# Kernel tuning notes

Hardware: AMD Instinct MI355X
Metric: run time of the kernel (lower is better)

The kernel has to match this reference:

```python
import jax, jax.numpy as jnp
import numpy as np

N = 100000      # nodes
E = 1600000     # edges
G = 2000        # molecules (graphs)
F = 40          # node features
FE = 16         # edge features
H = 64          # conv width
HM = 128        # mlp width
C = 2           # classes
NEG_SLOPE = 0.01
BN_EPS = 1e-5


def leaky(x):
    return jnp.where(x >= 0, x, NEG_SLOPE * x)


def batch_norm(x, g, b):
    # training-mode BatchNorm over the node axis (biased variance, eps=1e-5)
    m = jnp.mean(x, axis=0)
    v = jnp.var(x, axis=0)
    return (x - m) * jax.lax.rsqrt(v + BN_EPS) * g + b


def setup_inputs() -> dict:
    key = jax.random.key(0)
    ks = iter(jax.random.split(key, 100))

    def nrm(shape, s=1.0):
        return jax.random.normal(next(ks), shape, dtype=jnp.float32) * s

    inp = {}
    inp["x"] = nrm((N, F))
    inp["edge_index"] = jax.random.randint(next(ks), (2, E), 0, N, dtype=jnp.int32)
    inp["edge_attr"] = nrm((E, FE))
    inp["batch"] = jnp.repeat(jnp.arange(G, dtype=jnp.int32), N // G)

    dims = [(F, H), (H, H), (H, H)]
    for i, (ci, co) in enumerate(dims):
        inp[f"conv{i}_eps"] = jnp.zeros((1,), dtype=jnp.float32)
        inp[f"conv{i}_We"] = nrm((FE, ci), 1.0 / np.sqrt(FE))
        inp[f"conv{i}_be"] = nrm((ci,), 0.05)
        inp[f"conv{i}_W1"] = nrm((ci, co), 1.0 / np.sqrt(ci))
        inp[f"conv{i}_b1"] = nrm((co,), 0.05)
        inp[f"conv{i}_g1"] = 1.0 + nrm((co,), 0.05)
        inp[f"conv{i}_bt1"] = nrm((co,), 0.05)
        inp[f"conv{i}_W2"] = nrm((co, co), 1.0 / np.sqrt(co))
        inp[f"conv{i}_b2"] = nrm((co,), 0.05)
        inp[f"bn{i}_g"] = 1.0 + nrm((co,), 0.05)
        inp[f"bn{i}_b"] = nrm((co,), 0.05)

    inp["mlp0_W"] = nrm((2 * H, HM), 1.0 / np.sqrt(2 * H))
    inp["mlp0_b"] = nrm((HM,), 0.05)
    inp["mlp1_W"] = nrm((HM, HM), 1.0 / np.sqrt(HM))
    inp["mlp1_b"] = nrm((HM,), 0.05)
    inp["final_W"] = nrm((HM, C), 1.0 / np.sqrt(HM))
    inp["final_b"] = nrm((C,), 0.05)
    return inp


def _forward(x, edge_attr, edge_index, batch, convs, mlps, final_W, final_b):
    src, dst = edge_index[0], edge_index[1]
    for (eps, We, be, W1, b1, g1, bt1, W2, b2, bg, bb) in convs:
        # GINEConv: msg = relu(x_src + lin_edge(edge_attr)); scatter-add to dst
        e = edge_attr @ We + be                    # [E, in]
        msg = jax.nn.relu(x[src] + e)              # gather + fuse
        agg = jax.ops.segment_sum(msg, dst, num_segments=x.shape[0])
        h = (1.0 + eps) * x + agg
        # conv nn: Linear -> BatchNorm -> LeakyReLU -> Linear
        h = batch_norm(h @ W1 + b1, g1, bt1)
        h = leaky(h) @ W2 + b2
        # outer BatchNorm + LeakyReLU
        x = leaky(batch_norm(h, bg, bb))
    # global_add_pool then repeat_interleave by per-mol counts == pool[batch]
    pool = jax.ops.segment_sum(x, batch, num_segments=G)
    x = jnp.concatenate([x, pool[batch]], axis=1)  # [N, 2H]
    for (W, b) in mlps:
        x = leaky(x @ W + b)  # dropout is identity in eval mode
    return x @ final_W + final_b


def reference(x, edge_index, edge_attr, batch,
              conv0_eps, conv0_We, conv0_be, conv0_W1, conv0_b1, conv0_g1, conv0_bt1, conv0_W2, conv0_b2, bn0_g, bn0_b,
              conv1_eps, conv1_We, conv1_be, conv1_W1, conv1_b1, conv1_g1, conv1_bt1, conv1_W2, conv1_b2, bn1_g, bn1_b,
              conv2_eps, conv2_We, conv2_be, conv2_W1, conv2_b1, conv2_g1, conv2_bt1, conv2_W2, conv2_b2, bn2_g, bn2_b,
              mlp0_W, mlp0_b, mlp1_W, mlp1_b, final_W, final_b):
    convs = [
        (conv0_eps, conv0_We, conv0_be, conv0_W1, conv0_b1, conv0_g1, conv0_bt1, conv0_W2, conv0_b2, bn0_g, bn0_b),
        (conv1_eps, conv1_We, conv1_be, conv1_W1, conv1_b1, conv1_g1, conv1_bt1, conv1_W2, conv1_b2, bn1_g, bn1_b),
        (conv2_eps, conv2_We, conv2_be, conv2_W1, conv2_b1, conv2_g1, conv2_bt1, conv2_W2, conv2_b2, bn2_g, bn2_b),
    ]
    mlps = [(mlp0_W, mlp0_b), (mlp1_W, mlp1_b)]
    return _forward(x, edge_attr, edge_index, batch, convs, mlps, final_W, final_b)
```

## Files before the change

kernel.cpp:

```cpp
#include <hip/hip_runtime.h>


#define N_  100000
#define E_  1600000
#define G_  2000
#define SCAN_NB 196
#define NBLK 1563

__device__ __forceinline__ float leaky_(float z) { return z >= 0.f ? z : 0.01f * z; }

__global__ __launch_bounds__(256) void hist_kernel(
    const int* __restrict__ dst, int* __restrict__ cur)
{
    for (int e = blockIdx.x * 256 + threadIdx.x; e < E_; e += gridDim.x * 256)
        atomicAdd(&cur[dst[e]], 1);
}

__global__ __launch_bounds__(256) void scanA(
    const int* __restrict__ cur, int* __restrict__ blocksum)
{
    __shared__ int s[256];
    const int t = threadIdx.x, b = blockIdx.x;
    const int i0 = (b * 256 + t) * 2;
    int v = 0;
    if (i0 < N_) v += cur[i0];
    if (i0 + 1 < N_) v += cur[i0 + 1];
    s[t] = v; __syncthreads();
    for (int o = 128; o > 0; o >>= 1) { if (t < o) s[t] += s[t + o]; __syncthreads(); }
    if (t == 0) blocksum[b] = s[0];
}

__global__ __launch_bounds__(256) void scanB(
    const int* __restrict__ blocksum, int* __restrict__ blockpref)
{
    __shared__ int s[256];
    const int t = threadIdx.x;
    int v = (t < SCAN_NB) ? blocksum[t] : 0;
    s[t] = v; __syncthreads();
    for (int o = 1; o < 256; o <<= 1) {
        int u = (t >= o) ? s[t - o] : 0;
        __syncthreads(); s[t] += u; __syncthreads();
    }
    blockpref[t] = s[t] - v;
}

__global__ __launch_bounds__(256) void scanC(
    int* __restrict__ cur, int* __restrict__ off,
    const int* __restrict__ blockpref)
{
    __shared__ int s[256];
    const int t = threadIdx.x, b = blockIdx.x;
    const int i0 = (b * 256 + t) * 2;
    int v0 = (i0 < N_) ? cur[i0] : 0;
    int v1 = (i0 + 1 < N_) ? cur[i0 + 1] : 0;
    int pv = v0 + v1;
    s[t] = pv; __syncthreads();
    for (int o = 1; o < 256; o <<= 1) {
        int u = (t >= o) ? s[t - o] : 0;
        __syncthreads(); s[t] += u; __syncthreads();
    }
    int run = blockpref[b] + s[t] - pv;
    if (i0 < N_) {
        off[i0] = run; cur[i0] = run; run += v0;
        if (i0 + 1 < N_) { off[i0 + 1] = run; cur[i0 + 1] = run; }
    }
    if (b == 0 && t == 0) off[N_] = E_;
}

__global__ __launch_bounds__(256) void scatter_kernel(
    const int* __restrict__ src, const int* __restrict__ dst,
    int* __restrict__ cur, int* __restrict__ src_s, int* __restrict__ eid_s)
{
    for (int e = blockIdx.x * 256 + threadIdx.x; e < E_; e += gridDim.x * 256) {
        int p = atomicAdd(&cur[dst[e]], 1);
        src_s[p] = src[e];
        eid_s[p] = e;
    }
}

__global__ __launch_bounds__(256) void reorder_ea(
    const float* __restrict__ edge_attr, const int* __restrict__ eid_s,
    float4* __restrict__ ea_s)
{
    for (int t = blockIdx.x * 256 + threadIdx.x; t < E_ * 4; t += gridDim.x * 256) {
        int p = t >> 2, q = t & 3;
        int e = eid_s[p];
        ea_s[t] = ((const float4*)edge_attr)[e * 4 + q];
    }
}

#define DPW 13
#define CHUNK 32

template<int CI>
__global__ __launch_bounds__(256, 4) void agg_sorted(
    const float* __restrict__ ea_s,
    const int* __restrict__ src_s,
    const int* __restrict__ off,
    const float* __restrict__ We, const float* __restrict__ be,
    const float* __restrict__ x, float* __restrict__ agg)
{
    __shared__ __align__(16) float s_ea[4][2][CHUNK * 16];
    __shared__ int s_src[4][2][CHUNK];
    const int t = threadIdx.x;
    const int lane = t & 63;
    const int w = t >> 6;
    const int wid = __builtin_amdgcn_readfirstlane(blockIdx.x * 4 + w);

    float wcol[16];
#pragma unroll
    for (int k = 0; k < 16; ++k) wcol[k] = 0.f;
    float beL = 0.f;
    if (lane < CI) {
#pragma unroll
        for (int k = 0; k < 16; ++k) wcol[k] = We[k * CI + lane];
        beL = be[lane];
    }
    const int ln = (lane < CI) ? lane : 0;

    const int d0 = wid * DPW;
    if (d0 >= N_) return;
    const int d1 = min(d0 + DPW, N_);
    const int pw0 = off[d0];
    const int pw1 = off[d1];

    int d = d0;
    int e1 = off[d0 + 1];
    float acc = 0.f;
    int buf = 0;

    {
        const int m4 = min(CHUNK, pw1 - pw0) * 4;
#pragma unroll
        for (int j = 0; j < 2; ++j) {
            const int f = lane + 64 * j;
            float4 v = make_float4(0.f, 0.f, 0.f, 0.f);
            if (f < m4) v = *(const float4*)&ea_s[(size_t)pw0 * 16 + f * 4];
            *(float4*)&s_ea[w][0][f * 4] = v;
        }
        if (lane < CHUNK) {
            const int m = min(CHUNK, pw1 - pw0);
            s_src[w][0][lane] = (lane < m) ? src_s[pw0 + lane] : 0;
        }
    }
    __builtin_amdgcn_wave_barrier();

    for (int cp = pw0; cp < pw1; cp += CHUNK) {
        const int m = min(CHUNK, pw1 - cp);
        const int np = cp + CHUNK;
        const int nm = min(CHUNK, pw1 - np);

        float4 pre0 = make_float4(0.f, 0.f, 0.f, 0.f), pre1 = pre0;
        int psrc = 0;
        if (nm > 0) {
            { int f = lane;      if (f < nm * 4) pre0 = *(const float4*)&ea_s[(size_t)np * 16 + f * 4]; }
            { int f = lane + 64; if (f < nm * 4) pre1 = *(const float4*)&ea_s[(size_t)np * 16 + f * 4]; }
            if (lane < nm) psrc = src_s[np + lane];
        }

        float xr[CHUNK];
#pragma unroll
        for (int i = 0; i < CHUNK; ++i) {
            const int s = s_src[w][buf][i];
            xr[i] = x[(size_t)s * CI + ln];
        }

#pragma unroll
        for (int i = 0; i < CHUNK; ++i) {
            if (i >= m) break;
            while (cp + i == e1) {
                if (lane < CI) agg[(size_t)d * CI + lane] = acc;
                acc = 0.f; ++d;
                e1 = off[d + 1];
            }
            const float* er = &s_ea[w][buf][i * 16];
            float dotv = beL;
#pragma unroll
            for (int k = 0; k < 16; k += 4) {
                float4 ev = *(const float4*)&er[k];
                dotv += ev.x * wcol[k] + ev.y * wcol[k + 1]
                      + ev.z * wcol[k + 2] + ev.w * wcol[k + 3];
            }
            float mm = xr[i] + dotv;
            acc += (mm > 0.f ? mm : 0.f);
        }

        if (nm > 0) {
            *(float4*)&s_ea[w][buf ^ 1][lane * 4] = pre0;
            *(float4*)&s_ea[w][buf ^ 1][(lane + 64) * 4] = pre1;
            if (lane < CHUNK) s_src[w][buf ^ 1][lane] = psrc;
        }
        __builtin_amdgcn_wave_barrier();
        buf ^= 1;
    }

    while (d < d1) {
        if (lane < CI) agg[(size_t)d * CI + lane] = acc;
        acc = 0.f; ++d;
    }
}

template<int CI, int MODE>
__global__ __launch_bounds__(256, 4) void node_gemm(
    const float* __restrict__ in,
    const float* __restrict__ agg,
    const float* __restrict__ eps,
    const float* __restrict__ g1,
    const float* __restrict__ bt1,
    const float* __restrict__ stIn,
    const float* __restrict__ W, const float* __restrict__ bias_,
    float* __restrict__ outbuf, float* __restrict__ partial)
{
    __shared__ __align__(16) float a_lds[64][CI + 4];
    __shared__ __align__(16) float w_lds[CI][68];
    __shared__ float s_sc[64], s_sh[64];
    const int t = threadIdx.x;
    const int n0 = blockIdx.x * 64;
    constexpr int QR = CI / 4;

    if (MODE == 1) {
        if (t < 64) {
            float mean = stIn[t] * (1.0f / N_);
            float var  = stIn[64 + t] * (1.0f / N_) - mean * mean;
            float sc = g1[t] * rsqrtf(var + 1e-5f);
            s_sc[t] = sc;
            s_sh[t] = bt1[t] - mean * sc;
        }
        __syncthreads();
    }

    if (MODE == 0) {
        const float hs = 1.0f + eps[0];
        for (int f = t; f < 64 * QR; f += 256) {
            int i = f / QR, q = f - i * QR;
            int n = n0 + i;
            float4 val = make_float4(0.f, 0.f, 0.f, 0.f);
            if (n < N_) {
                float4 xa = *(const float4*)&in[(size_t)n * CI + q * 4];
                float4 ag = *(const float4*)&agg[(size_t)n * CI + q * 4];
                val = make_float4(hs * xa.x + ag.x, hs * xa.y + ag.y,
                                  hs * xa.z + ag.z, hs * xa.w + ag.w);
            }
            *(float4*)&a_lds[i][q * 4] = val;
        }
    } else {
        for (int f = t; f < 64 * QR; f += 256) {
            int i = f / QR, q = f - i * QR;
            int n = n0 + i;
            float4 val = make_float4(0.f, 0.f, 0.f, 0.f);
            if (n < N_) {
                float4 uv = *(const float4*)&in[(size_t)n * CI + q * 4];
                int c = q * 4;
                val = make_float4(leaky_(uv.x * s_sc[c]     + s_sh[c]),
                                  leaky_(uv.y * s_sc[c + 1] + s_sh[c + 1]),
                                  leaky_(uv.z * s_sc[c + 2] + s_sh[c + 2]),
                                  leaky_(uv.w * s_sc[c + 3] + s_sh[c + 3]));
            }
            *(float4*)&a_lds[i][q * 4] = val;
        }
    }
    for (int f = t; f < CI * 16; f += 256) {
        int k = f >> 4, cq = f & 15;
        *(float4*)&w_lds[k][cq * 4] = *(const float4*)&W[k * 64 + cq * 4];
    }
    __syncthreads();

    const int tr = t & 15;
    const int c0 = (t >> 4) * 4;
    float acc[4][4] = {};
#pragma unroll 2
    for (int k = 0; k < CI; k += 4) {
        float ar[4][4];
#pragma unroll
        for (int j = 0; j < 4; ++j)
            *(float4*)&ar[j][0] = *(const float4*)&a_lds[tr + 16 * j][k];
#pragma unroll
        for (int kk = 0; kk < 4; ++kk) {
            float4 b = *(const float4*)&w_lds[k + kk][c0];
#pragma unroll
            for (int j = 0; j < 4; ++j) {
                acc[j][0] += ar[j][kk] * b.x;
                acc[j][1] += ar[j][kk] * b.y;
                acc[j][2] += ar[j][kk] * b.z;
                acc[j][3] += ar[j][kk] * b.w;
            }
        }
    }

    const float4 bb = *(const float4*)&bias_[c0];
    const float bias[4] = { bb.x, bb.y, bb.z, bb.w };
    float ls[4] = {}, lq[4] = {};
#pragma unroll
    for (int j = 0; j < 4; ++j) {
        int n = n0 + tr + 16 * j;
        if (n < N_) {
            float o[4];
#pragma unroll
            for (int cc = 0; cc < 4; ++cc) {
                o[cc] = acc[j][cc] + bias[cc];
                ls[cc] += o[cc];
                lq[cc] += o[cc] * o[cc];
            }
            *(float4*)&outbuf[(size_t)n * 64 + c0] = make_float4(o[0], o[1], o[2], o[3]);
        }
    }
#pragma unroll
    for (int m = 1; m <= 8; m <<= 1) {
#pragma unroll
        for (int cc = 0; cc < 4; ++cc) {
            ls[cc] += __shfl_xor(ls[cc], m);
            lq[cc] += __shfl_xor(lq[cc], m);
        }
    }
    if (tr == 0) {
#pragma unroll
        for (int cc = 0; cc < 4; ++cc) {
            partial[(size_t)(c0 + cc) * NBLK + blockIdx.x]      = ls[cc];
            partial[(size_t)(64 + c0 + cc) * NBLK + blockIdx.x] = lq[cc];
        }
    }
}

__global__ __launch_bounds__(256) void finalize_stats(
    const float* __restrict__ partial, float* __restrict__ stats)
{
    const int c = blockIdx.x;
    const int t = threadIdx.x;
    float s = 0.f;
    for (int b = t; b < NBLK; b += 256) s += partial[(size_t)c * NBLK + b];
    __shared__ float red[256];
    red[t] = s; __syncthreads();
    for (int o = 128; o > 0; o >>= 1) { if (t < o) red[t] += red[t + o]; __syncthreads(); }
    if (t == 0) stats[c] = red[0];
}

__global__ __launch_bounds__(256) void apply_bn_leaky(
    const float* __restrict__ v, const float* __restrict__ st,
    const float* __restrict__ g, const float* __restrict__ b,
    float* __restrict__ xout)
{
    size_t idx = ((size_t)blockIdx.x * 256 + threadIdx.x) * 4;
    if (idx >= (size_t)N_ * 64) return;
    int c0 = (int)(idx & 63);
    float4 vv = *(const float4*)&v[idx];
    float vi[4] = { vv.x, vv.y, vv.z, vv.w };
    float o[4];
#pragma unroll
    for (int cc = 0; cc < 4; ++cc) {
        int c = c0 + cc;
        float mean = st[c] * (1.0f / N_);
        float var  = st[64 + c] * (1.0f / N_) - mean * mean;
        float sc = g[c] * rsqrtf(var + 1e-5f);
        float sh = b[c] - mean * sc;
        o[cc] = leaky_(vi[cc] * sc + sh);
    }
    *(float4*)&xout[idx] = make_float4(o[0], o[1], o[2], o[3]);
}

__global__ __launch_bounds__(256) void pool_kernel(
    const float* __restrict__ x, float* __restrict__ pool)
{
    const int c = threadIdx.x & 63;
    const int g = blockIdx.x * 4 + (threadIdx.x >> 6);
    const float* p = x + (size_t)g * 50 * 64 + c;
    float s = 0.f;
#pragma unroll
    for (int j = 0; j < 50; ++j) s += p[(size_t)j * 64];
    pool[(size_t)g * 64 + c] = s;
}

__global__ __launch_bounds__(256) void pool_mlp0(
    const float* __restrict__ pool, const float* __restrict__ W0,
    const float* __restrict__ b0, float* __restrict__ g0)
{
    const int t = threadIdx.x;
    const int g = blockIdx.x * 2 + (t >> 7);
    const int c = t & 127;
    float s = b0[c];
    const float* pr = pool + (size_t)g * 64;
#pragma unroll 4
    for (int k = 0; k < 64; ++k)
        s += pr[k] * W0[(size_t)(64 + k) * 128 + c];
    g0[(size_t)g * 128 + c] = s;
}

__global__ __launch_bounds__(256, 2) void mlp_kernel(
    const float* __restrict__ x, const float* __restrict__ g0,
    const float* __restrict__ W0,
    const float* __restrict__ W1, const float* __restrict__ b1,
    const float* __restrict__ Wf, const float* __restrict__ bf,
    float* __restrict__ out)
{
    __shared__ __align__(16) float a_lds[128][132];
    __shared__ __align__(16) float w_lds[16][132];
    __shared__ __align__(16) float sWfT[2][128];
    __shared__ int sbid[128];
    const int t = threadIdx.x;
    const int n0 = blockIdx.x * 128;

    for (int f = t; f < 128 * 16; f += 256) {
        int i = f >> 4, q = f & 15;
        int n = n0 + i;
        float4 val = make_float4(0.f, 0.f, 0.f, 0.f);
        if (n < N_) val = *(const float4*)&x[(size_t)n * 64 + q * 4];
        *(float4*)&a_lds[i][q * 4] = val;
    }
    if (t < 128) {
        int n = n0 + t;
        sbid[t] = (n < N_) ? (n / 50) : (G_ - 1);
        sWfT[0][t] = Wf[t * 2];
        sWfT[1][t] = Wf[t * 2 + 1];
    }

    const int tr = t & 15;
    const int c0 = (t >> 4) * 8;
    float acc[8][8];

#pragma unroll
    for (int j = 0; j < 8; ++j)
#pragma unroll
        for (int cc = 0; cc < 8; ++cc) acc[j][cc] = 0.f;

    for (int kc = 0; kc < 64; kc += 16) {
        __syncthreads();
        for (int f = t; f < 16 * 32; f += 256) {
            int k = f >> 5, cq = f & 31;
            *(float4*)&w_lds[k][cq * 4] = *(const float4*)&W0[(size_t)(kc + k) * 128 + cq * 4];
        }
        __syncthreads();
        for (int k = 0; k < 16; k += 4) {
            float ar[8][4];
#pragma unroll
            for (int j = 0; j < 8; ++j)
                *(float4*)&ar[j][0] = *(const float4*)&a_lds[tr + 16 * j][kc + k];
#pragma unroll
            for (int kk = 0; kk < 4; ++kk) {
                float4 bA = *(const float4*)&w_lds[k + kk][c0];
                float4 bB = *(const float4*)&w_lds[k + kk][c0 + 4];
#pragma unroll
                for (int j = 0; j < 8; ++j) {
                    acc[j][0] += ar[j][kk] * bA.x;
                    acc[j][1] += ar[j][kk] * bA.y;
                    acc[j][2] += ar[j][kk] * bA.z;
                    acc[j][3] += ar[j][kk] * bA.w;
                    acc[j][4] += ar[j][kk] * bB.x;
                    acc[j][5] += ar[j][kk] * bB.y;
                    acc[j][6] += ar[j][kk] * bB.z;
                    acc[j][7] += ar[j][kk] * bB.w;
                }
            }
        }
    }
    __syncthreads();
#pragma unroll
    for (int j = 0; j < 8; ++j) {
        int row = tr + 16 * j;
        const float* gr = g0 + (size_t)sbid[row] * 128;
        float4 gA = *(const float4*)&gr[c0];
        float4 gB = *(const float4*)&gr[c0 + 4];
        float o[8] = { acc[j][0] + gA.x, acc[j][1] + gA.y, acc[j][2] + gA.z, acc[j][3] + gA.w,
                       acc[j][4] + gB.x, acc[j][5] + gB.y, acc[j][6] + gB.z, acc[j][7] + gB.w };
#pragma unroll
        for (int cc = 0; cc < 8; ++cc) o[cc] = leaky_(o[cc]);
        *(float4*)&a_lds[row][c0]     = make_float4(o[0], o[1], o[2], o[3]);
        *(float4*)&a_lds[row][c0 + 4] = make_float4(o[4], o[5], o[6], o[7]);
    }

#pragma unroll
    for (int j = 0; j < 8; ++j)
#pragma unroll
        for (int cc = 0; cc < 8; ++cc) acc[j][cc] = 0.f;

    for (int kc = 0; kc < 128; kc += 16) {
        __syncthreads();
        for (int f = t; f < 16 * 32; f += 256) {
            int k = f >> 5, cq = f & 31;
            *(float4*)&w_lds[k][cq * 4] = *(const float4*)&W1[(size_t)(kc + k) * 128 + cq * 4];
        }
        __syncthreads();
        for (int k = 0; k < 16; k += 4) {
            float ar[8][4];
#pragma unroll
            for (int j = 0; j < 8; ++j)
                *(float4*)&ar[j][0] = *(const float4*)&a_lds[tr + 16 * j][kc + k];
#pragma unroll
            for (int kk = 0; kk < 4; ++kk) {
                float4 bA = *(const float4*)&w_lds[k + kk][c0];
                float4 bB = *(const float4*)&w_lds[k + kk][c0 + 4];
#pragma unroll
                for (int j = 0; j < 8; ++j) {
                    acc[j][0] += ar[j][kk] * bA.x;
                    acc[j][1] += ar[j][kk] * bA.y;
                    acc[j][2] += ar[j][kk] * bA.z;
                    acc[j][3] += ar[j][kk] * bA.w;
                    acc[j][4] += ar[j][kk] * bB.x;
                    acc[j][5] += ar[j][kk] * bB.y;
                    acc[j][6] += ar[j][kk] * bB.z;
                    acc[j][7] += ar[j][kk] * bB.w;
                }
            }
        }
    }
    __syncthreads();
    {
        float4 bb0 = *(const float4*)&b1[c0];
        float4 bb1 = *(const float4*)&b1[c0 + 4];
        float bias[8] = { bb0.x, bb0.y, bb0.z, bb0.w, bb1.x, bb1.y, bb1.z, bb1.w };
#pragma unroll
        for (int j = 0; j < 8; ++j) {
            int row = tr + 16 * j;
            float o[8];
#pragma unroll
            for (int cc = 0; cc < 8; ++cc) o[cc] = leaky_(acc[j][cc] + bias[cc]);
            *(float4*)&a_lds[row][c0]     = make_float4(o[0], o[1], o[2], o[3]);
            *(float4*)&a_lds[row][c0 + 4] = make_float4(o[4], o[5], o[6], o[7]);
        }
    }
    __syncthreads();

    {
        int i = t >> 1, c = t & 1;
        int n = n0 + i;
        if (n < N_) {
            float s = bf[c];
            for (int k = 0; k < 128; k += 4) {
                float4 av = *(const float4*)&a_lds[i][k];
                float4 wv = *(const float4*)&sWfT[c][k];
                s += av.x * wv.x + av.y * wv.y + av.z * wv.z + av.w * wv.w;
            }
            out[(size_t)n * 2 + c] = s;
        }
    }
}

extern "C" void kernel_launch(void* const* d_in, const int* in_sizes, int n_in,
                              void* d_out, int out_size, void* d_ws, size_t ws_size,
                              hipStream_t stream)
{
    (void)in_sizes; (void)n_in; (void)out_size; (void)ws_size;

    const float* x0    = (const float*)d_in[0];
    const int*   eidx  = (const int*)d_in[1];
    const float* eattr = (const float*)d_in[2];
    const float* L[3][11];
    for (int l = 0; l < 3; ++l)
        for (int j = 0; j < 11; ++j)
            L[l][j] = (const float*)d_in[4 + l * 11 + j];
    const float* mlp0W = (const float*)d_in[37];
    const float* mlp0b = (const float*)d_in[38];
    const float* mlp1W = (const float*)d_in[39];
    const float* mlp1b = (const float*)d_in[40];
    const float* finW  = (const float*)d_in[41];
    const float* finb  = (const float*)d_in[42];
    float* out = (float*)d_out;

    float* ws    = (float*)d_ws;
    float* agg   = ws;
    float* u     = agg  + (size_t)N_ * 64;
    float* xbuf  = u    + (size_t)N_ * 64;
    float* pool  = xbuf + (size_t)N_ * 64;
    float* g0    = pool + (size_t)G_ * 64;
    float* stats = g0   + (size_t)G_ * 128;
    float* partial = stats + 768;
    int*   off   = (int*)(partial + 128 * NBLK);
    int*   cur   = off + (N_ + 1);
    int*   bsum  = cur + N_;
    int*   bpref = bsum + 256;
    int*   src_s = bpref + 256;
    float* ea_s  = (float*)(src_s + E_);
    int*   eid_s = (int*)xbuf;
    float* v = agg;

    const int* src = eidx;
    const int* dst = eidx + E_;
    const int GB = NBLK;

    hipMemsetAsync(cur, 0, (size_t)N_ * sizeof(int), stream);
    hist_kernel<<<2048, 256, 0, stream>>>(dst, cur);
    scanA<<<SCAN_NB, 256, 0, stream>>>(cur, bsum);
    scanB<<<1, 256, 0, stream>>>(bsum, bpref);
    scanC<<<SCAN_NB, 256, 0, stream>>>(cur, off, bpref);
    scatter_kernel<<<2048, 256, 0, stream>>>(src, dst, cur, src_s, eid_s);
    reorder_ea<<<2048, 256, 0, stream>>>(eattr, eid_s, (float4*)ea_s);

    const int AGGB = ((N_ + DPW - 1) / DPW + 3) / 4 + 1;

    for (int l = 0; l < 3; ++l) {
        float* s1 = stats + (2 * l) * 128;
        float* s2 = stats + (2 * l + 1) * 128;
        if (l == 0) {
            agg_sorted<40><<<AGGB, 256, 0, stream>>>(ea_s, src_s, off, L[0][1], L[0][2], x0, agg);
            node_gemm<40, 0><<<GB, 256, 0, stream>>>(x0, agg, L[0][0], nullptr, nullptr, nullptr,
                                                     L[0][3], L[0][4], u, partial);
        } else {
            agg_sorted<64><<<AGGB, 256, 0, stream>>>(ea_s, src_s, off, L[l][1], L[l][2], xbuf, agg);
            node_gemm<64, 0><<<GB, 256, 0, stream>>>(xbuf, agg, L[l][0], nullptr, nullptr, nullptr,
                                                     L[l][3], L[l][4], u, partial);
        }
        finalize_stats<<<128, 256, 0, stream>>>(partial, s1);
        node_gemm<64, 1><<<GB, 256, 0, stream>>>(u, nullptr, nullptr, L[l][5], L[l][6], s1,
                                                 L[l][7], L[l][8], v, partial);
        finalize_stats<<<128, 256, 0, stream>>>(partial, s2);
        apply_bn_leaky<<<6250, 256, 0, stream>>>(v, s2, L[l][9], L[l][10], xbuf);
    }

    pool_kernel<<<G_ / 4, 256, 0, stream>>>(xbuf, pool);
    pool_mlp0<<<G_ / 2, 256, 0, stream>>>(pool, mlp0W, mlp0b, g0);
    mlp_kernel<<<(N_ + 127) / 128, 256, 0, stream>>>(xbuf, g0, mlp0W,
                                                     mlp1W, mlp1b, finW, finb, out);
}
```

Measured before the change: 1.077 ms.

## Record edge ranks in histogram pass and fuse scatter with edge-attr reorder

The histogram kernel now stores each edge's atomic rank, so the placement pass computes its slot as off[dst]+rank with no second round of atomics. Placement and the edge-attribute reorder become one kernel that reads each edge's 16 floats contiguously and writes them to the sorted slot, which removes the eid_s buffer and its extra read. The trade is a rank array (E ints) written and read back, and edge_attr rows now land as scattered 64-byte writes instead of gathered reads. Separately, agg_sorted's occupancy hint rises from 4 to 8 blocks per CU, which may force the compiler to spill registers.

```diff
diff --git a/kernel.cpp b/kernel.cpp
--- a/kernel.cpp
+++ b/kernel.cpp
@@ -9,22 +9,23 @@
 
 __device__ __forceinline__ float leaky_(float z) { return z >= 0.f ? z : 0.01f * z; }
 
-__global__ __launch_bounds__(256) void hist_kernel(
-    const int* __restrict__ dst, int* __restrict__ cur)
-{
+__global__ __launch_bounds__(256) void hist_rank_kernel(
+    const int* __restrict__ dst, int* __restrict__ cnt, int* __restrict__ rank)
+{
+#pragma unroll 4
     for (int e = blockIdx.x * 256 + threadIdx.x; e < E_; e += gridDim.x * 256)
-        atomicAdd(&cur[dst[e]], 1);
+        rank[e] = atomicAdd(&cnt[dst[e]], 1);
 }
 
 __global__ __launch_bounds__(256) void scanA(
-    const int* __restrict__ cur, int* __restrict__ blocksum)
+    const int* __restrict__ cnt, int* __restrict__ blocksum)
 {
     __shared__ int s[256];
     const int t = threadIdx.x, b = blockIdx.x;
     const int i0 = (b * 256 + t) * 2;
     int v = 0;
-    if (i0 < N_) v += cur[i0];
-    if (i0 + 1 < N_) v += cur[i0 + 1];
+    if (i0 < N_) v += cnt[i0];
+    if (i0 + 1 < N_) v += cnt[i0 + 1];
     s[t] = v; __syncthreads();
     for (int o = 128; o > 0; o >>= 1) { if (t < o) s[t] += s[t + o]; __syncthreads(); }
     if (t == 0) blocksum[b] = s[0];
@@ -45,14 +46,14 @@
 }
 
 __global__ __launch_bounds__(256) void scanC(
-    int* __restrict__ cur, int* __restrict__ off,
+    const int* __restrict__ cnt, int* __restrict__ off,
     const int* __restrict__ blockpref)
 {
     __shared__ int s[256];
     const int t = threadIdx.x, b = blockIdx.x;
     const int i0 = (b * 256 + t) * 2;
-    int v0 = (i0 < N_) ? cur[i0] : 0;
-    int v1 = (i0 + 1 < N_) ? cur[i0 + 1] : 0;
+    int v0 = (i0 < N_) ? cnt[i0] : 0;
+    int v1 = (i0 + 1 < N_) ? cnt[i0 + 1] : 0;
     int pv = v0 + v1;
     s[t] = pv; __syncthreads();
     for (int o = 1; o < 256; o <<= 1) {
@@ -61,31 +62,26 @@
     }
     int run = blockpref[b] + s[t] - pv;
     if (i0 < N_) {
-        off[i0] = run; cur[i0] = run; run += v0;
-        if (i0 + 1 < N_) { off[i0 + 1] = run; cur[i0 + 1] = run; }
+        off[i0] = run; run += v0;
+        if (i0 + 1 < N_) off[i0 + 1] = run;
     }
     if (b == 0 && t == 0) off[N_] = E_;
 }
 
-__global__ __launch_bounds__(256) void scatter_kernel(
+__global__ __launch_bounds__(256) void place_kernel(
     const int* __restrict__ src, const int* __restrict__ dst,
-    int* __restrict__ cur, int* __restrict__ src_s, int* __restrict__ eid_s)
-{
+    const int* __restrict__ rank, const int* __restrict__ off,
+    const float* __restrict__ edge_attr,
+    int* __restrict__ src_s, float* __restrict__ ea_s)
+{
+#pragma unroll 2
     for (int e = blockIdx.x * 256 + threadIdx.x; e < E_; e += gridDim.x * 256) {
-        int p = atomicAdd(&cur[dst[e]], 1);
+        const int p = off[dst[e]] + rank[e];
         src_s[p] = src[e];
-        eid_s[p] = e;
-    }
-}
-
-__global__ __launch_bounds__(256) void reorder_ea(
-    const float* __restrict__ edge_attr, const int* __restrict__ eid_s,
-    float4* __restrict__ ea_s)
-{
-    for (int t = blockIdx.x * 256 + threadIdx.x; t < E_ * 4; t += gridDim.x * 256) {
-        int p = t >> 2, q = t & 3;
-        int e = eid_s[p];
-        ea_s[t] = ((const float4*)edge_attr)[e * 4 + q];
+        const float4* __restrict__ ea = (const float4*)(edge_attr + (size_t)e * 16);
+        float4* __restrict__ eo = (float4*)(ea_s + (size_t)p * 16);
+        float4 a0 = ea[0], a1 = ea[1], a2 = ea[2], a3 = ea[3];
+        eo[0] = a0; eo[1] = a1; eo[2] = a2; eo[3] = a3;
     }
 }
 
@@ -93,7 +89,7 @@
 #define CHUNK 32
 
 template<int CI>
-__global__ __launch_bounds__(256, 4) void agg_sorted(
+__global__ __launch_bounds__(256, 8) void agg_sorted(
     const float* __restrict__ ea_s,
     const int* __restrict__ src_s,
     const int* __restrict__ off,
@@ -130,18 +126,16 @@
     int buf = 0;
 
     {
-        const int m4 = min(CHUNK, pw1 - pw0) * 4;
+        const int m = min(CHUNK, pw1 - pw0);
 #pragma unroll
         for (int j = 0; j < 2; ++j) {
             const int f = lane + 64 * j;
             float4 v = make_float4(0.f, 0.f, 0.f, 0.f);
-            if (f < m4) v = *(const float4*)&ea_s[(size_t)pw0 * 16 + f * 4];
+            if (f < m * 4) v = *(const float4*)&ea_s[(size_t)pw0 * 16 + f * 4];
             *(float4*)&s_ea[w][0][f * 4] = v;
         }
-        if (lane < CHUNK) {
-            const int m = min(CHUNK, pw1 - pw0);
+        if (lane < CHUNK)
             s_src[w][0][lane] = (lane < m) ? src_s[pw0 + lane] : 0;
-        }
     }
     __builtin_amdgcn_wave_barrier();
 
@@ -563,25 +557,24 @@
     float* stats = g0   + (size_t)G_ * 128;
     float* partial = stats + 768;
     int*   off   = (int*)(partial + 128 * NBLK);
-    int*   cur   = off + (N_ + 1);
-    int*   bsum  = cur + N_;
+    int*   cnt   = off + (N_ + 2);
+    int*   bsum  = cnt + N_;
     int*   bpref = bsum + 256;
-    int*   src_s = bpref + 256;
-    float* ea_s  = (float*)(src_s + E_);
-    int*   eid_s = (int*)xbuf;
+    int*   rank  = bpref + 256;
+    int*   src_s = rank + E_;
+    float* ea_s  = (float*)((((uintptr_t)(src_s + E_)) + 63) & ~(uintptr_t)63);
     float* v = agg;
 
     const int* src = eidx;
     const int* dst = eidx + E_;
     const int GB = NBLK;
 
-    hipMemsetAsync(cur, 0, (size_t)N_ * sizeof(int), stream);
-    hist_kernel<<<2048, 256, 0, stream>>>(dst, cur);
-    scanA<<<SCAN_NB, 256, 0, stream>>>(cur, bsum);
+    hipMemsetAsync(cnt, 0, (size_t)N_ * sizeof(int), stream);
+    hist_rank_kernel<<<2048, 256, 0, stream>>>(dst, cnt, rank);
+    scanA<<<SCAN_NB, 256, 0, stream>>>(cnt, bsum);
     scanB<<<1, 256, 0, stream>>>(bsum, bpref);
-    scanC<<<SCAN_NB, 256, 0, stream>>>(cur, off, bpref);
-    scatter_kernel<<<2048, 256, 0, stream>>>(src, dst, cur, src_s, eid_s);
-    reorder_ea<<<2048, 256, 0, stream>>>(eattr, eid_s, (float4*)ea_s);
+    scanC<<<SCAN_NB, 256, 0, stream>>>(cnt, off, bpref);
+    place_kernel<<<2048, 256, 0, stream>>>(src, dst, rank, off, eattr, src_s, ea_s);
 
     const int AGGB = ((N_ + DPW - 1) / DPW + 3) / 4 + 1;
 
```

Measured after the change: 1.346 ms. 1.25x slower.
